# Kernel tuning notes

Hardware: AMD Instinct MI355X
Metric: run time of the kernel (lower is better)

Reference implementation:

```python
import jax, jax.numpy as jnp
import numpy as np

EMB = 768
HEADS = 12
DK = EMB // HEADS


def setup_inputs() -> dict:
    key = jax.random.key(0)
    ks = jax.random.split(key, 11)
    B, S = 2, 2048
    lim = 1.0 / np.sqrt(EMB)
    def lin(k):
        kw, kb = jax.random.split(k)
        W = jax.random.uniform(kw, (EMB, EMB), jnp.float32, -lim, lim)
        b = jax.random.uniform(kb, (EMB,), jnp.float32, -lim, lim)
        return W, b
    Wq, bq = lin(ks[0])
    Wk, bk = lin(ks[1])
    Wv, bv = lin(ks[2])
    Wo, bo = lin(ks[3])
    return {
        "query": jax.random.normal(ks[4], (B, S, EMB), jnp.float32),
        "key": jax.random.normal(ks[5], (B, S, EMB), jnp.float32),
        "value": jax.random.normal(ks[6], (B, S, EMB), jnp.float32),
        "Wq": Wq, "bq": bq, "Wk": Wk, "bk": bk,
        "Wv": Wv, "bv": bv, "Wo": Wo, "bo": bo,
    }


def reference(query, key, value, Wq, bq, Wk, bk, Wv, bv, Wo, bo):
    B, S, _ = query.shape
    # nn.Linear: x @ W^T + b, then split heads -> [B, H, S, d_k]
    def proj(x, W, b):
        return (x @ W.T + b).reshape(B, -1, HEADS, DK).transpose(0, 2, 1, 3)
    q = proj(query, Wq, bq)
    k = proj(key, Wk, bk)
    v = proj(value, Wv, bv)
    scale = 1.0 / jnp.sqrt(jnp.float32(DK))
    scores = jnp.einsum('bhqd,bhkd->bhqk', q, k) * scale  # [B,H,S,S]
    attn = jax.nn.softmax(scores, axis=-1)
    av = jnp.einsum('bhqk,bhkd->bhqd', attn, v)
    concat = av.transpose(0, 2, 1, 3).reshape(B, -1, EMB)
    return concat @ Wo.T + bo
```

## Files before the change

### kernel.cpp

```cpp
#include <hip/hip_runtime.h>
#include <hip/hip_bf16.h>

#define EMB 768
#define HEADS 12
#define DKV 64
#define BATCH 2
#define SEQ 2048
#define NTOK (BATCH*SEQ)

typedef float f32x4 __attribute__((ext_vector_type(4)));
typedef unsigned short u16;
typedef u16 u16x8 __attribute__((ext_vector_type(8)));
typedef u16 u16x4 __attribute__((ext_vector_type(4)));
typedef __bf16 bf16x8 __attribute__((ext_vector_type(8)));

__device__ __forceinline__ u16 f2bf(float f) {
  return __builtin_bit_cast(u16, (__bf16)f);
}
__device__ __forceinline__ float fexp2(float x) {
#if __has_builtin(__builtin_amdgcn_exp2f)
  return __builtin_amdgcn_exp2f(x);
#else
  return exp2f(x);
#endif
}
__device__ __forceinline__ f32x4 mfma16(u16x8 a, u16x8 b, f32x4 c) {
  return __builtin_amdgcn_mfma_f32_16x16x32_bf16(
      __builtin_bit_cast(bf16x8, a), __builtin_bit_cast(bf16x8, b), c, 0, 0, 0);
}
__device__ __forceinline__ void gload16(const void* g, void* l) {
  __builtin_amdgcn_global_load_lds(
      (const __attribute__((address_space(1))) void*)g,
      (__attribute__((address_space(3))) void*)l, 16, 0, 0);
}

__global__ void cast_w_k(
    const float* __restrict__ w0, const float* __restrict__ w1,
    const float* __restrict__ w2, const float* __restrict__ w3,
    u16* __restrict__ W0, u16* __restrict__ W1, u16* __restrict__ W2, u16* __restrict__ W3)
{
  const int NW = EMB*EMB/8;
  int i = blockIdx.x*256 + threadIdx.x;
  if (i >= 4*NW) return;
  int which = i / NW, off = i - which*NW;
  const float* s = which==0 ? w0 : which==1 ? w1 : which==2 ? w2 : w3;
  u16* d        = which==0 ? W0 : which==1 ? W1 : which==2 ? W2 : W3;
  float4 a = reinterpret_cast<const float4*>(s)[off*2];
  float4 b = reinterpret_cast<const float4*>(s)[off*2+1];
  u16x8 o;
  o[0]=f2bf(a.x); o[1]=f2bf(a.y); o[2]=f2bf(a.z); o[3]=f2bf(a.w);
  o[4]=f2bf(b.x); o[5]=f2bf(b.y); o[6]=f2bf(b.z); o[7]=f2bf(b.w);
  reinterpret_cast<u16x8*>(d)[off] = o;
}

template<int MODE, bool AF32>
__device__ __forceinline__ void gemm_core(
    const void* __restrict__ Ap, const u16* __restrict__ Bm,
    const float* __restrict__ bias, float ascale, float bscale,
    void* __restrict__ outp, u16* __restrict__ At, u16* __restrict__ Bt,
    int m0, int n0)
{
  const int t = threadIdx.x;
  const int w = t >> 6, lane = t & 63, lg = lane >> 4, lr = lane & 15;
  const int wr = w >> 1, wc = w & 1;
  const int lrow = lane >> 3, csl = lane & 7;

  f32x4 acc[2][4] = {};
  f32x4 raf[2][2];

  auto A_LOAD = [&](int kb) {
    #pragma unroll
    for (int q2 = 0; q2 < 2; ++q2) {
      int c = q2*256 + t, row = c >> 3, sl = c & 7;
      const float* p = (const float*)Ap + (size_t)(m0+row)*EMB + kb + sl*8;
      raf[q2][0] = *reinterpret_cast<const f32x4*>(p);
      raf[q2][1] = *reinterpret_cast<const f32x4*>(p + 4);
    }
  };
  auto A_WRITE = [&]() {
    #pragma unroll
    for (int q2 = 0; q2 < 2; ++q2) {
      int c = q2*256 + t, row = c >> 3, sl = c & 7;
      u16x8 v;
      #pragma unroll
      for (int j = 0; j < 4; ++j) {
        v[j]   = f2bf(raf[q2][0][j] * ascale);
        v[4+j] = f2bf(raf[q2][1][j] * ascale);
      }
      *reinterpret_cast<u16x8*>(&At[row*64 + ((sl ^ (row & 7))*8)]) = v;
    }
  };
  auto A_GLOAD = [&](int kb) {
    #pragma unroll
    for (int i = 0; i < 2; ++i) {
      int ci = w*2 + i;
      int row = ci*8 + lrow;
      int sg = csl ^ (row & 7);
      gload16((const u16*)Ap + (size_t)(m0+row)*EMB + kb + sg*8, &At[ci*512]);
    }
  };
  auto B_GLOAD = [&](int kb) {
    #pragma unroll
    for (int i = 0; i < 4; ++i) {
      int ci = w*4 + i;
      int row = ci*8 + lrow;
      int sg = csl ^ (row & 7);
      gload16(Bm + (size_t)(n0+row)*EMB + kb + sg*8, &Bt[ci*512]);
    }
  };

  auto COMPUTE = [&]() {
    u16x8 af[2][2], bf[4][2];
    #pragma unroll
    for (int fm = 0; fm < 2; ++fm)
      #pragma unroll
      for (int kk = 0; kk < 2; ++kk) {
        int r = wr*32 + fm*16 + lr;
        int p = (lg + 4*kk) ^ (r & 7);
        af[fm][kk] = *reinterpret_cast<const u16x8*>(&At[r*64 + p*8]);
      }
    #pragma unroll
    for (int fn = 0; fn < 4; ++fn)
      #pragma unroll
      for (int kk = 0; kk < 2; ++kk) {
        int r = wc*64 + fn*16 + lr;
        int p = (lg + 4*kk) ^ (r & 7);
        bf[fn][kk] = *reinterpret_cast<const u16x8*>(&Bt[r*64 + p*8]);
      }
    __builtin_amdgcn_s_setprio(1);
    #pragma unroll
    for (int fm = 0; fm < 2; ++fm)
      #pragma unroll
      for (int fn = 0; fn < 4; ++fn)
        #pragma unroll
        for (int kk = 0; kk < 2; ++kk)
          acc[fm][fn] = mfma16(af[fm][kk], bf[fn][kk], acc[fm][fn]);
    __builtin_amdgcn_s_setprio(0);
  };

  const int NSTEP = EMB/64;
  if constexpr (AF32) {
    A_LOAD(0);
    B_GLOAD(0);
    A_WRITE();
    __syncthreads();
    #pragma unroll
    for (int ts = 0; ts < NSTEP; ++ts) {
      if (ts+1 < NSTEP) A_LOAD((ts+1)*64);
      COMPUTE();
      if (ts+1 < NSTEP) {
        __syncthreads();
        B_GLOAD((ts+1)*64);
        A_WRITE();
        __syncthreads();
      }
    }
  } else {
    #pragma unroll
    for (int ts = 0; ts < NSTEP; ++ts) {
      A_GLOAD(ts*64);
      B_GLOAD(ts*64);
      __syncthreads();
      COMPUTE();
      if (ts+1 < NSTEP) __syncthreads();
    }
  }

  #pragma unroll
  for (int fm = 0; fm < 2; ++fm)
    #pragma unroll
    for (int fn = 0; fn < 4; ++fn) {
      const int mb = m0 + wr*32 + fm*16 + lg*4;
      const int e  = n0 + wc*64 + fn*16 + lr;
      if constexpr (MODE == 2) {
        int bb = mb >> 11, sb = mb & 2047, h = e >> 6, d = e & 63;
        u16x4 o4;
        #pragma unroll
        for (int j = 0; j < 4; ++j) o4[j] = f2bf(acc[fm][fn][j] + bias[e]*bscale);
        *reinterpret_cast<u16x4*>(
            reinterpret_cast<u16*>(outp) + (((size_t)(bb*HEADS+h))*DKV + d)*SEQ + sb) = o4;
      } else {
        #pragma unroll
        for (int j = 0; j < 4; ++j) {
          int m = mb + j;
          float val = acc[fm][fn][j] + bias[e]*bscale;
          if constexpr (MODE == 0) {
            int bb = m >> 11, s = m & 2047, h = e >> 6, d = e & 63;
            reinterpret_cast<u16*>(outp)[(((size_t)(bb*HEADS+h))*SEQ + s)*DKV + d] = f2bf(val);
          } else {
            reinterpret_cast<float*>(outp)[(size_t)m*EMB + e] = val;
          }
        }
      }
    }
}

__global__ __launch_bounds__(256) void qkv_k(
    const float* __restrict__ Xq, const float* __restrict__ Xk, const float* __restrict__ Xv,
    const u16* __restrict__ Wq, const u16* __restrict__ Wk, const u16* __restrict__ Wv,
    const float* __restrict__ bq, const float* __restrict__ bk, const float* __restrict__ bv,
    u16* __restrict__ Qh, u16* __restrict__ Kh, u16* __restrict__ Vh, float csc)
{
  __shared__ __align__(16) u16 At[64*64];
  __shared__ __align__(16) u16 Bt[128*64];
  const int m0 = blockIdx.x*64, n0 = blockIdx.y*128;
  const int z = blockIdx.z;
  if (z == 0)
    gemm_core<0,true>(Xq, Wq, bq, csc, csc, Qh, At, Bt, m0, n0);
  else if (z == 1)
    gemm_core<0,true>(Xk, Wk, bk, 1.f, 1.f, Kh, At, Bt, m0, n0);
  else
    gemm_core<2,true>(Xv, Wv, bv, 1.f, 1.f, Vh, At, Bt, m0, n0);
}

__global__ __launch_bounds__(256) void gemm_out_k(
    const u16* __restrict__ A, const u16* __restrict__ Bm,
    const float* __restrict__ bias, float* __restrict__ outp)
{
  __shared__ __align__(16) u16 At[64*64];
  __shared__ __align__(16) u16 Bt[128*64];
  gemm_core<1,false>(A, Bm, bias, 1.f, 1.f, outp, At, Bt, blockIdx.x*64, blockIdx.y*128);
}

__global__ __launch_bounds__(256) void flash_attn_k(
    const u16* __restrict__ Q, const u16* __restrict__ K, const u16* __restrict__ VT,
    u16* __restrict__ av)
{
  __shared__ __align__(16) u16 Kt[2][64*64];
  __shared__ __align__(16) u16 Vt[2][64*64];
  __shared__ __align__(16) u16 Pt[4][16*64];

  const int t = threadIdx.x;
  const int w = t >> 6, lane = t & 63, lg = lane >> 4, lr = lane & 15;
  const int qb = blockIdx.x;
  const int bh = blockIdx.y;
  const u16* Qb = Q  + (size_t)bh*SEQ*DKV;
  const u16* Kb = K  + (size_t)bh*SEQ*DKV;
  const u16* Vb = VT + (size_t)bh*DKV*SEQ;

  const int qrow = qb*64 + w*16 + lr;
  u16x8 qf[2];
  qf[0] = *reinterpret_cast<const u16x8*>(Qb + (size_t)qrow*DKV + lg*8);
  qf[1] = *reinterpret_cast<const u16x8*>(Qb + (size_t)qrow*DKV + 32 + lg*8);

  f32x4 acc[4] = {};
  float mrun = -1e30f, lrun = 0.f;

  auto STAGE = [&](int kt0, int bi) {
    #pragma unroll
    for (int c2 = 0; c2 < 2; ++c2) {
      int c = c2*256 + t;
      int row = c >> 3, sl = c & 7;
      int sg = sl ^ (row & 7);
      gload16(Kb + (size_t)(kt0+row)*DKV + sg*8, &Kt[bi][c*8]);
    }
    #pragma unroll
    for (int c2 = 0; c2 < 2; ++c2) {
      int c = c2*256 + t;
      int row = c >> 3, sl = c & 7;
      int sg = sl ^ (row & 7);
      gload16(Vb + (size_t)row*SEQ + kt0 + sg*8, &Vt[bi][c*8]);
    }
  };

  const int NT = SEQ/64;
  char* Pw = reinterpret_cast<char*>(&Pt[w][0]);

#define TILE(bi, kt)                                                          \
  do {                                                                        \
    if ((kt)+1 < NT) STAGE(((kt)+1)*64, (bi)^1);    \
    f32x4 s[4];                                                               \
    __builtin_amdgcn_s_setprio(1);                                            \
    _Pragma("unroll")                                                         \
    for (int fc = 0; fc < 4; ++fc) {                                          \
      f32x4 z = {};                                                           \
      _Pragma("unroll")                                                       \
      for (int kk = 0; kk < 2; ++kk) {                                        \
        int r = fc*16 + lr;                                                   \
        int slot = (lg + 4*kk) ^ (r & 7);                                     \
        u16x8 kf = *reinterpret_cast<const u16x8*>(&Kt[bi][r*64 + slot*8]);   \
        z = mfma16(kf, qf[kk], z);                                            \
      }                                                                       \
      s[fc] = z;                                                              \
    }                                                                         \
    __builtin_amdgcn_s_setprio(0);                                            \
    float a0 = fmaxf(fmaxf(s[0][0], s[0][1]), s[0][2]);                       \
    float a1 = fmaxf(fmaxf(s[0][3], s[1][0]), s[1][1]);                       \
    float a2 = fmaxf(fmaxf(s[1][2], s[1][3]), s[2][0]);                       \
    float a3 = fmaxf(fmaxf(s[2][1], s[2][2]), s[2][3]);                       \
    float a4 = fmaxf(fmaxf(s[3][0], s[3][1]), s[3][2]);                       \
    float pmax = fmaxf(fmaxf(fmaxf(a0, a1), a2),                              \
                       fmaxf(fmaxf(a3, a4), s[3][3]));                        \
    if (__any(pmax > mrun + 8.f)) {          \
      float pm = fmaxf(pmax, __shfl_xor(pmax, 16));                           \
      pm = fmaxf(pm, __shfl_xor(pm, 32));                                     \
      float mnew = fmaxf(mrun, pm);                                           \
      float corr = fexp2(mrun - mnew);                                        \
      mrun = mnew; lrun *= corr;                                              \
      _Pragma("unroll")                                                       \
      for (int fc = 0; fc < 4; ++fc)                                          \
        _Pragma("unroll")                                                     \
        for (int j = 0; j < 4; ++j)                                           \
          acc[fc][j] *= corr;                                                 \
    }                                                                         \
    float p[4][4], rs[4];                                                     \
    _Pragma("unroll")                                                         \
    for (int fc = 0; fc < 4; ++fc) {                                          \
      _Pragma("unroll")                                                       \
      for (int j = 0; j < 4; ++j) p[fc][j] = fexp2(s[fc][j] - mrun);          \
      rs[fc] = (p[fc][0] + p[fc][1]) + (p[fc][2] + p[fc][3]);                 \
    }                                                                         \
    lrun += (rs[0] + rs[1]) + (rs[2] + rs[3]);      \
    _Pragma("unroll")                                                         \
    for (int fc = 0; fc < 4; ++fc) {                                          \
      u16x4 q4;                                                               \
      _Pragma("unroll")                                                       \
      for (int j = 0; j < 4; ++j) q4[j] = f2bf(p[fc][j]);                     \
      *reinterpret_cast<u16x4*>(                                              \
          Pw + lr*128 + (((fc*4 + lg) ^ ((lr & 7) << 1))*8)) = q4;            \
    }                                                                         \
    asm volatile("s_waitcnt lgkmcnt(0)" ::: "memory");                        \
    __builtin_amdgcn_sched_barrier(0);                                        \
    __builtin_amdgcn_s_setprio(1);                                            \
    _Pragma("unroll")                                                         \
    for (int kk = 0; kk < 2; ++kk) {                                          \
      u16x8 pf = *reinterpret_cast<const u16x8*>(                             \
          Pw + lr*128 + (((kk*8 + lg*2) ^ ((lr & 7) << 1))*8));               \
      _Pragma("unroll")                                                       \
      for (int fc = 0; fc < 4; ++fc) {                                        \
        int rv = fc*16 + lr;                                                  \
        int slotv = (lg + 4*kk) ^ (rv & 7);                                   \
        u16x8 vf = *reinterpret_cast<const u16x8*>(&Vt[bi][rv*64 + slotv*8]); \
        acc[fc] = mfma16(vf, pf, acc[fc]);                                    \
      }                                                                       \
    }                                                                         \
    __builtin_amdgcn_s_setprio(0);                                            \
    __syncthreads();   \
  } while (0)

  STAGE(0, 0);
  __syncthreads();
  for (int kt = 0; kt < NT; kt += 2) {
    TILE(0, kt);
    TILE(1, kt+1);
  }
#undef TILE

  float lt = lrun;
  lt += __shfl_xor(lt, 16);
  lt += __shfl_xor(lt, 32);
  const float inv = 1.0f / lt;

  const int b = bh / HEADS, h = bh % HEADS;
  #pragma unroll
  for (int fc = 0; fc < 4; ++fc) {
    u16x4 o4;
    #pragma unroll
    for (int j = 0; j < 4; ++j) o4[j] = f2bf(acc[fc][j] * inv);
    *reinterpret_cast<u16x4*>(
        av + ((size_t)(b*SEQ + qrow))*EMB + h*64 + fc*16 + lg*4) = o4;
  }
}

extern "C" void kernel_launch(void* const* d_in, const int* in_sizes, int n_in,
                              void* d_out, int out_size, void* d_ws, size_t ws_size,
                              hipStream_t stream) {
  const float* xq_f = (const float*)d_in[0];
  const float* xk_f = (const float*)d_in[1];
  const float* xv_f = (const float*)d_in[2];
  const float* Wq = (const float*)d_in[3];
  const float* bq = (const float*)d_in[4];
  const float* Wk = (const float*)d_in[5];
  const float* bk = (const float*)d_in[6];
  const float* Wv = (const float*)d_in[7];
  const float* bv = (const float*)d_in[8];
  const float* Wo = (const float*)d_in[9];
  const float* bo = (const float*)d_in[10];

  const size_t NX = (size_t)NTOK*EMB;
  const size_t NW = (size_t)EMB*EMB;
  u16* Wc0 = (u16*)d_ws;
  u16* Wc1 = Wc0 + NW;
  u16* Wc2 = Wc1 + NW;
  u16* Wc3 = Wc2 + NW;
  u16* Qh  = Wc3 + NW;
  u16* Kh  = Qh + NX;
  u16* Vh  = Kh + NX;
  u16* Xb  = Vh + NX;

  const float csc = 0.125f * 1.4426950408889634f;

  cast_w_k<<<dim3(4*EMB*EMB/8/256), dim3(256), 0, stream>>>(
      Wq, Wk, Wv, Wo, Wc0, Wc1, Wc2, Wc3);

  qkv_k<<<dim3(NTOK/64, EMB/128, 3), dim3(256), 0, stream>>>(
      xq_f, xk_f, xv_f, Wc0, Wc1, Wc2, bq, bk, bv, Qh, Kh, Vh, csc);

  flash_attn_k<<<dim3(SEQ/64, BATCH*HEADS), dim3(256), 0, stream>>>(Qh, Kh, Vh, Xb);

  gemm_out_k<<<dim3(NTOK/64, EMB/128), dim3(256), 0, stream>>>(Xb, Wc3, bo, (float*)d_out);
}
```

Baseline: 96.01 us.

## Double-buffer LDS tiles in projection GEMMs to overlap loads with MFMA

New measurement: 95.66 us. About the same (-0.4%).

```diff
diff --git a/kernel.cpp b/kernel.cpp
--- a/kernel.cpp
+++ b/kernel.cpp
@@ -77,7 +77,7 @@
       raf[q2][1] = *reinterpret_cast<const f32x4*>(p + 4);
     }
   };
-  auto A_WRITE = [&]() {
+  auto A_WRITE = [&](int bi) {
     #pragma unroll
     for (int q2 = 0; q2 < 2; ++q2) {
       int c = q2*256 + t, row = c >> 3, sl = c & 7;
@@ -87,29 +87,30 @@
         v[j]   = f2bf(raf[q2][0][j] * ascale);
         v[4+j] = f2bf(raf[q2][1][j] * ascale);
       }
-      *reinterpret_cast<u16x8*>(&At[row*64 + ((sl ^ (row & 7))*8)]) = v;
-    }
-  };
-  auto A_GLOAD = [&](int kb) {
+      *reinterpret_cast<u16x8*>(&At[bi*4096 + row*64 + ((sl ^ (row & 7))*8)]) = v;
+    }
+  };
+  auto A_GLOAD = [&](int kb, int bi) {
     #pragma unroll
     for (int i = 0; i < 2; ++i) {
       int ci = w*2 + i;
       int row = ci*8 + lrow;
       int sg = csl ^ (row & 7);
-      gload16((const u16*)Ap + (size_t)(m0+row)*EMB + kb + sg*8, &At[ci*512]);
-    }
-  };
-  auto B_GLOAD = [&](int kb) {
+      gload16((const u16*)Ap + (size_t)(m0+row)*EMB + kb + sg*8,
+              &At[bi*4096 + ci*512]);
+    }
+  };
+  auto B_GLOAD = [&](int kb, int bi) {
     #pragma unroll
     for (int i = 0; i < 4; ++i) {
       int ci = w*4 + i;
       int row = ci*8 + lrow;
       int sg = csl ^ (row & 7);
-      gload16(Bm + (size_t)(n0+row)*EMB + kb + sg*8, &Bt[ci*512]);
-    }
-  };
-
-  auto COMPUTE = [&]() {
+      gload16(Bm + (size_t)(n0+row)*EMB + kb + sg*8, &Bt[bi*8192 + ci*512]);
+    }
+  };
+
+  auto COMPUTE = [&](int bi) {
     u16x8 af[2][2], bf[4][2];
     #pragma unroll
     for (int fm = 0; fm < 2; ++fm)
@@ -117,7 +118,7 @@
       for (int kk = 0; kk < 2; ++kk) {
         int r = wr*32 + fm*16 + lr;
         int p = (lg + 4*kk) ^ (r & 7);
-        af[fm][kk] = *reinterpret_cast<const u16x8*>(&At[r*64 + p*8]);
+        af[fm][kk] = *reinterpret_cast<const u16x8*>(&At[bi*4096 + r*64 + p*8]);
       }
     #pragma unroll
     for (int fn = 0; fn < 4; ++fn)
@@ -125,7 +126,7 @@
       for (int kk = 0; kk < 2; ++kk) {
         int r = wc*64 + fn*16 + lr;
         int p = (lg + 4*kk) ^ (r & 7);
-        bf[fn][kk] = *reinterpret_cast<const u16x8*>(&Bt[r*64 + p*8]);
+        bf[fn][kk] = *reinterpret_cast<const u16x8*>(&Bt[bi*8192 + r*64 + p*8]);
       }
     __builtin_amdgcn_s_setprio(1);
     #pragma unroll
@@ -141,27 +142,32 @@
   const int NSTEP = EMB/64;
   if constexpr (AF32) {
     A_LOAD(0);
-    B_GLOAD(0);
-    A_WRITE();
+    B_GLOAD(0, 0);
+    A_WRITE(0);
     __syncthreads();
     #pragma unroll
     for (int ts = 0; ts < NSTEP; ++ts) {
-      if (ts+1 < NSTEP) A_LOAD((ts+1)*64);
-      COMPUTE();
       if (ts+1 < NSTEP) {
+        A_LOAD((ts+1)*64);
+        B_GLOAD((ts+1)*64, (ts & 1) ^ 1);
+      }
+      COMPUTE(ts & 1);
+      if (ts+1 < NSTEP) {
+        A_WRITE((ts & 1) ^ 1);
         __syncthreads();
-        B_GLOAD((ts+1)*64);
-        A_WRITE();
-        __syncthreads();
       }
     }
   } else {
+    A_GLOAD(0, 0);
+    B_GLOAD(0, 0);
+    __syncthreads();
     #pragma unroll
     for (int ts = 0; ts < NSTEP; ++ts) {
-      A_GLOAD(ts*64);
-      B_GLOAD(ts*64);
-      __syncthreads();
-      COMPUTE();
+      if (ts+1 < NSTEP) {
+        A_GLOAD((ts+1)*64, (ts & 1) ^ 1);
+        B_GLOAD((ts+1)*64, (ts & 1) ^ 1);
+      }
+      COMPUTE(ts & 1);
       if (ts+1 < NSTEP) __syncthreads();
     }
   }
@@ -201,8 +207,8 @@
     const float* __restrict__ bq, const float* __restrict__ bk, const float* __restrict__ bv,
     u16* __restrict__ Qh, u16* __restrict__ Kh, u16* __restrict__ Vh, float csc)
 {
-  __shared__ __align__(16) u16 At[64*64];
-  __shared__ __align__(16) u16 Bt[128*64];
+  __shared__ __align__(16) u16 At[2*64*64];
+  __shared__ __align__(16) u16 Bt[2*128*64];
   const int m0 = blockIdx.x*64, n0 = blockIdx.y*128;
   const int z = blockIdx.z;
   if (z == 0)
@@ -217,8 +223,8 @@
     const u16* __restrict__ A, const u16* __restrict__ Bm,
     const float* __restrict__ bias, float* __restrict__ outp)
 {
-  __shared__ __align__(16) u16 At[64*64];
-  __shared__ __align__(16) u16 Bt[128*64];
+  __shared__ __align__(16) u16 At[2*64*64];
+  __shared__ __align__(16) u16 Bt[2*128*64];
   gemm_core<1,false>(A, Bm, bias, 1.f, 1.f, outp, At, Bt, blockIdx.x*64, blockIdx.y*128);
 }
 
```
